# Performance work log

Hardware: AMD Instinct MI355X
Metric: run time of the kernel (lower is better)

Reference implementation:

```python
import jax, jax.numpy as jnp
import numpy as np

B, T, D_MODEL = 2, 2048, 2048
N_HEAD, N_KV = 16, 4
HEAD_DIM = D_MODEL // N_HEAD  # 128
N_REP = N_HEAD // N_KV        # 4
ROPE_BASE = 10000.0


def setup_inputs() -> dict:
    key = jax.random.key(0)
    ks = jax.random.split(key, 5)
    s = 0.02
    return {
        "x": jax.random.normal(ks[0], (B, T, D_MODEL), dtype=jnp.float32),
        "Wq": jax.random.normal(ks[1], (D_MODEL, N_HEAD * HEAD_DIM), dtype=jnp.float32) * s,
        "Wk": jax.random.normal(ks[2], (D_MODEL, N_KV * HEAD_DIM), dtype=jnp.float32) * s,
        "Wv": jax.random.normal(ks[3], (D_MODEL, N_KV * HEAD_DIM), dtype=jnp.float32) * s,
        "Wo": jax.random.normal(ks[4], (D_MODEL, D_MODEL), dtype=jnp.float32) * s,
    }


def _rope_cos_sin(seq_len, dim, dtype):
    inv_freq = 1.0 / (ROPE_BASE ** (jnp.arange(0, dim, 2, dtype=jnp.float32) / dim))
    t = jnp.arange(seq_len, dtype=jnp.float32)
    freqs = t[:, None] * inv_freq[None, :]          # (T, dim/2)
    emb = jnp.concatenate([freqs, freqs], axis=-1)  # (T, dim)
    return jnp.cos(emb).astype(dtype), jnp.sin(emb).astype(dtype)


def _rotate_half(x):
    half = x.shape[-1] // 2
    return jnp.concatenate([-x[..., half:], x[..., :half]], axis=-1)


def reference(x, Wq, Wk, Wv, Wo):
    Bx, Tx, _ = x.shape
    # projections (weights stored (in, out); equals torch Linear with W^T)
    q = (x @ Wq).reshape(Bx, Tx, N_HEAD, HEAD_DIM).transpose(0, 2, 1, 3)  # (B,H,T,d)
    k = (x @ Wk).reshape(Bx, Tx, N_KV, HEAD_DIM).transpose(0, 2, 1, 3)    # (B,Hkv,T,d)
    v = (x @ Wv).reshape(Bx, Tx, N_KV, HEAD_DIM).transpose(0, 2, 1, 3)

    cos, sin = _rope_cos_sin(Tx, HEAD_DIM, x.dtype)  # (T, d)
    q = q * cos + _rotate_half(q) * sin
    k = k * cos + _rotate_half(k) * sin

    # grouped attention: q grouped by kv head, avoids materializing repeated K/V
    qg = q.reshape(Bx, N_KV, N_REP, Tx, HEAD_DIM)
    scale = 1.0 / np.sqrt(HEAD_DIM)
    att = jnp.einsum('bgrtd,bgsd->bgrts', qg, k) * scale  # (B,Hkv,rep,T,S)
    causal = jnp.tril(jnp.ones((Tx, Tx), dtype=bool))
    att = jnp.where(causal, att, -jnp.inf)
    att = jax.nn.softmax(att, axis=-1)
    y = jnp.einsum('bgrts,bgsd->bgrtd', att, v)           # (B,Hkv,rep,T,d)
    y = y.reshape(Bx, N_HEAD, Tx, HEAD_DIM).transpose(0, 2, 1, 3).reshape(Bx, Tx, D_MODEL)
    return y @ Wo
```

## Files before the change

### kernel.cpp

```cpp
#include <hip/hip_runtime.h>
#include <hip/hip_bf16.h>

typedef unsigned short u16;
typedef unsigned int u32;
typedef __attribute__((ext_vector_type(4))) float f32x4;
typedef __attribute__((ext_vector_type(8))) __bf16 bf16x8;

#define B_   2
#define T_   2048
#define DM   2048
#define NH   16
#define NKV  4
#define HD   128

__device__ __forceinline__ u16 f2bf(float f){
    u32 u = __builtin_bit_cast(u32, f);
    u += 0x7FFFu + ((u >> 16) & 1u);
    return (u16)(u >> 16);
}
__device__ __forceinline__ float bf2f(u16 v){
    return __builtin_bit_cast(float, (u32)v << 16);
}

__device__ __forceinline__ float ex2(float x){
    float r; asm("v_exp_f32 %0, %1" : "=v"(r) : "v"(x)); return r;
}

__device__ __forceinline__ void gld_lds16(const void* g, void* l){
    __builtin_amdgcn_global_load_lds(
        (const __attribute__((address_space(1))) void*)g,
        (__attribute__((address_space(3))) void*)l, 16, 0, 0);
}

__global__ void prep(const float* __restrict__ x,
                     const float* __restrict__ Wq, const float* __restrict__ Wk,
                     const float* __restrict__ Wv, const float* __restrict__ Wo,
                     u16* __restrict__ xb, u16* __restrict__ Wqkv, u16* __restrict__ Wot,
                     float2* __restrict__ tab){
    __shared__ float tile[32][33];
    int bid = blockIdx.x, tid = threadIdx.x;
    if (bid < 8192){
        int i = bid * 256 + tid;
        float4 v = ((const float4*)x)[i];
        ushort4 o;
        o.x = f2bf(v.x); o.y = f2bf(v.y); o.z = f2bf(v.z); o.w = f2bf(v.w);
        ((ushort4*)xb)[i] = o;
    } else if (bid < 18432){
        int tb = bid - 8192;
        int bx = tb % 160, byy = tb / 160;
        const float* W; u16* Out; int N; int nb; int perm;
        if (bx < 64)      { W = Wq; Out = Wqkv;                  N = 2048; nb = bx;      perm = 1; }
        else if (bx < 80) { W = Wk; Out = Wqkv + 2048ull * 2048; N = 512;  nb = bx - 64; perm = 1; }
        else if (bx < 96) { W = Wv; Out = Wqkv + 2560ull * 2048; N = 512;  nb = bx - 80; perm = 0; }
        else              { W = Wo; Out = Wot;                   N = 2048; nb = bx - 96; perm = 0; }
        int n0 = nb * 32, k0 = byy * 32;
        int tx = tid & 31, ty = tid >> 5;
#pragma unroll
        for (int i = 0; i < 4; i++)
            tile[ty + i * 8][tx] = W[(size_t)(k0 + ty + i * 8) * N + n0 + tx];
        __syncthreads();
#pragma unroll
        for (int i = 0; i < 4; i++){
            int n = n0 + ty + i * 8;
            int np = perm ? ((n & ~127) | ((n & 63) << 1) | ((n >> 6) & 1)) : n;
            Out[(size_t)np * 2048 + k0 + tx] = f2bf(tile[tx][ty + i * 8]);
        }
    } else {
        int idx = (bid - 18432) * 256 + tid;
        int i = idx & 63, t = idx >> 6;
        float ang = (float)t * exp2f((float)i * (-13.287712379549449f / 64.0f));
        float sv, cv;
        __sincosf(ang, &sv, &cv);
        tab[idx] = make_float2(cv, sv);
    }
}

#define BARR() asm volatile("s_barrier" ::: "memory")
#define VM0()  asm volatile("s_waitcnt vmcnt(0)" ::: "memory")
#define VM4()  asm volatile("s_waitcnt vmcnt(4)" ::: "memory")
#define VM8()  asm volatile("s_waitcnt vmcnt(8)" ::: "memory")
#define VM10() asm volatile("s_waitcnt vmcnt(10)" ::: "memory")

__global__ __launch_bounds__(256, 2) void gemm192h(const u16* __restrict__ A, const u16* __restrict__ Bt,
                                                   u16* __restrict__ Qp, u16* __restrict__ Ktl,
                                                   u16* __restrict__ Vtl, const float2* __restrict__ tab){
    __shared__ __attribute__((aligned(16))) u16 As[2][8192];
    __shared__ __attribute__((aligned(16))) u16 Bs[2][12288];
    const int tid = threadIdx.x;
    const int lane = tid & 63, w = tid >> 6;
    const int wm = w >> 1, wn = w & 1;
    const int tg = lane >> 4, lx = lane & 15;
    int swz = ((int)blockIdx.x & 7) * 64 + ((int)blockIdx.x >> 3);
    const int bx = swz & 15, by = swz >> 4;
    const int m0 = by * 128, n0 = bx * 192;
    const int K = 2048;
    const int kcx = (lane & 7) ^ ((lane >> 3) & 7);

    f32x4 acc[4][6];
    const f32x4 Z = {0.f, 0.f, 0.f, 0.f};
#pragma unroll
    for (int i = 0; i < 4; i++)
#pragma unroll
        for (int j = 0; j < 6; j++) acc[i][j] = Z;
    bf16x8 a_[4][2], b_[2][2];

    auto stA2 = [&](int buf, int h, int kt){
#pragma unroll
        for (int l = 0; l < 2; l++){
            int rb = h * 64 + w * 16 + l * 8;
            gld_lds16(A + (size_t)(m0 + rb + (lane >> 3)) * K + kt * 64 + kcx * 8,
                      &As[buf][rb * 64 + lane * 8]);
        }
    };
    auto stB2 = [&](int buf, int cp, int kt){
#pragma unroll
        for (int l = 0; l < 2; l++){
            int rb = l * 96 + cp * 32 + w * 8;
            gld_lds16(Bt + (size_t)(n0 + rb + (lane >> 3)) * K + kt * 64 + kcx * 8,
                      &Bs[buf][rb * 64 + lane * 8]);
        }
    };

#define RA192(BUF) { \
    const char* ab = (const char*)&As[BUF][0]; \
    _Pragma("unroll") for (int mi = 0; mi < 4; mi++){ \
        int rh = wm*64 + mi*16 + lx; \
        _Pragma("unroll") for (int ks = 0; ks < 2; ks++) \
            a_[mi][ks] = *(const bf16x8*)(ab + rh*128 + (((ks*4+tg)*16) ^ ((lx&7)<<4))); \
    } }
#define RB192(BUF, C) { \
    const char* bb = (const char*)&Bs[BUF][0]; \
    _Pragma("unroll") for (int n = 0; n < 2; n++){ \
        int rb = wn*96 + (C)*32 + n*16 + lx; \
        _Pragma("unroll") for (int ks = 0; ks < 2; ks++) \
            b_[n][ks] = *(const bf16x8*)(bb + rb*128 + (((ks*4+tg)*16) ^ ((lx&7)<<4))); \
    } }
#define MM192(C) { \
    __builtin_amdgcn_s_setprio(1); \
    _Pragma("unroll") for (int mi = 0; mi < 4; mi++) \
    _Pragma("unroll") for (int n = 0; n < 2; n++) \
    _Pragma("unroll") for (int ks = 0; ks < 2; ks++) \
        acc[mi][(C)*2+n] = __builtin_amdgcn_mfma_f32_16x16x32_bf16( \
            a_[mi][ks], b_[n][ks], acc[mi][(C)*2+n], 0, 0, 0); \
    __builtin_amdgcn_s_setprio(0); }

    stA2(0, 0, 0); stA2(0, 1, 0); stB2(0, 0, 0); stB2(0, 1, 0); stB2(0, 2, 0);
    stA2(1, 0, 1); stA2(1, 1, 1); stB2(1, 0, 1); stB2(1, 1, 1);
    VM8(); BARR();

#pragma unroll 1
    for (int it = 0; it < 16; it++){
        const int O  = 2*it + 1;
        const int E2 = (2*it + 2 < 32) ? 2*it + 2 : 31;
        const int O2 = (2*it + 3 < 32) ? 2*it + 3 : 31;
        RA192(0); RB192(0, 0); stB2(1, 2, O);
        BARR(); MM192(0); BARR();
        RB192(0, 1); stA2(0, 0, E2); stB2(0, 0, E2);
        BARR(); MM192(1); BARR();
        RB192(0, 2); stA2(0, 1, E2); stB2(0, 1, E2);
        BARR(); MM192(2); VM10(); BARR();
        RA192(1); RB192(1, 0); stB2(0, 2, E2);
        BARR(); MM192(0); BARR();
        RB192(1, 1); stA2(1, 0, O2); stB2(1, 0, O2);
        BARR(); MM192(1); BARR();
        RB192(1, 2); stA2(1, 1, O2); stB2(1, 1, O2);
        BARR(); MM192(2); VM10(); BARR();
    }

    const float QS = 0.08838834764831845f * 1.4426950408889634f;
#pragma unroll
    for (int mi = 0; mi < 4; mi++){
        int r0 = m0 + wm*64 + mi*16 + tg*4;
#pragma unroll
        for (int ci = 0; ci < 6; ci++){
            int cb = n0 + wn*96 + ci*16;
            int c  = cb + lx;
            if (cb < 2048){
                int ii = (c & 127) >> 1;
#pragma unroll
                for (int j = 0; j < 4; j++){
                    float v = acc[mi][ci][j];
                    float p = __shfl_xor(v, 1);
                    int t = (r0 + j) & 2047;
                    float2 cs = tab[t * 64 + ii];
                    float o = ((lx & 1) ? (v * cs.x + p * cs.y) : (v * cs.x - p * cs.y)) * QS;
                    Qp[(size_t)(r0 + j) * 2048 + c] = f2bf(o);
                }
            } else if (cb < 2560){
                int hk = (c >> 7) & 3;
                int dd = c & 127;
                int ii = dd >> 1;
#pragma unroll
                for (int j = 0; j < 4; j++){
                    int r = r0 + j;
                    int bb2 = r >> 11, tt = r & 2047;
                    float v = acc[mi][ci][j];
                    float p = __shfl_xor(v, 1);
                    float2 cs = tab[tt * 64 + ii];
                    float o = (lx & 1) ? (v * cs.x + p * cs.y) : (v * cs.x - p * cs.y);
                    size_t tb = ((size_t)(bb2 * 4 + hk) * 32 + (tt >> 6)) * 8192;
                    u32 byte = (u32)((tt & 63) * 256) + (((u32)(2 * dd)) ^ ((u32)((tt & 7) << 4)));
                    Ktl[tb + byte / 2] = f2bf(o);
                }
            } else {
                int bb2 = r0 >> 11, ss = r0 & 2047;
                int sb = ss & 63;
                int hk = (c >> 7) & 3;
                int d  = c & 127;
                size_t tb = ((size_t)(bb2 * 4 + hk) * 32 + (ss >> 6)) * 8192;
                u32 swzd = (u32)((d & 7) << 4);
#pragma unroll
                for (int j = 0; j < 4; j++){
                    int s = sb + j;
                    int slot = (s & 32) | (((s >> 2) & 3) << 3) | (((s >> 4) & 1) << 2) | (s & 3);
                    u32 byte = (u32)(d * 128) + (((u32)(2 * slot)) ^ swzd);
                    Vtl[tb + byte / 2] = f2bf(acc[mi][ci][j]);
                }
            }
        }
    }
}
#undef RA192
#undef RB192
#undef MM192

#define READ_A(QA, BUF) { \
    const char* ab = (const char*)&As[BUF][wm][0]; \
    _Pragma("unroll") for (int i = 0; i < 4; i++){ \
        int rh = ((QA)*4 + i)*16 + lx; \
        _Pragma("unroll") for (int ks = 0; ks < 2; ks++) \
            a_[i][ks] = *(const bf16x8*)(ab + rh*128 + (((ks*4+tg)*16) ^ ((lx&7)<<4))); \
    } }
#define READ_B(QB, BUF) { \
    const char* bb = (const char*)&Bs[BUF][wn>>1][0]; \
    _Pragma("unroll") for (int n = 0; n < 2; n++){ \
        int rbh = (wn&1)*64 + ((QB)*2+n)*16 + lx; \
        _Pragma("unroll") for (int ks = 0; ks < 2; ks++) \
            b_[(QB)*2+n][ks] = *(const bf16x8*)(bb + rbh*128 + (((ks*4+tg)*16) ^ ((lx&7)<<4))); \
    } }
#define MFMA_Q(QA, QB) { \
    __builtin_amdgcn_s_setprio(1); \
    _Pragma("unroll") for (int i = 0; i < 4; i++) \
    _Pragma("unroll") for (int n = 0; n < 2; n++) \
    _Pragma("unroll") for (int ks = 0; ks < 2; ks++) \
        acc[(QA)*4+i][(QB)*2+n] = __builtin_amdgcn_mfma_f32_16x16x32_bf16( \
            a_[i][ks], b_[(QB)*2+n][ks], acc[(QA)*4+i][(QB)*2+n], 0, 0, 0); \
    __builtin_amdgcn_s_setprio(0); }

__global__ __launch_bounds__(512, 2) void gemmWo(const u16* __restrict__ A, const u16* __restrict__ Bt,
                                                 u16* __restrict__ O0){
    __shared__ __attribute__((aligned(16))) u16 As[2][2][8192];
    __shared__ __attribute__((aligned(16))) u16 Bs[2][2][8192];
    const int tid = threadIdx.x;
    const int lane = tid & 63, w = tid >> 6;
    const int wm = w >> 2, wn = w & 3;
    const int tg = lane >> 4, lx = lane & 15;
    int q8 = (int)gridDim.x >> 3;
    int swz = ((int)blockIdx.x & 7) * q8 + ((int)blockIdx.x >> 3);
    int kh = swz >> 7; swz &= 127;
    const int bx = swz & 7, by = swz >> 3;
    const int m0 = by * 256, n0 = bx * 256;
    const int K = 2048;
    const int NIT = 8;
    const int kt0 = kh * 16;
    const int ltMax = 2 * NIT - 1;
    const int kcx = (lane & 7) ^ ((lane >> 3) & 7);

    f32x4 acc[8][4];
    const f32x4 Z = {0.f, 0.f, 0.f, 0.f};
#pragma unroll
    for (int i = 0; i < 8; i++)
#pragma unroll
        for (int j = 0; j < 4; j++) acc[i][j] = Z;
    bf16x8 a_[4][2], b_[4][2];

    auto stA = [&](int buf, int q, int kt){
        int mh = w >> 2;
        int s0 = (w & 3) * 2;
#pragma unroll
        for (int l = 0; l < 2; l++){
            int s = s0 + l;
            gld_lds16(A + (size_t)(m0 + mh*128 + q*64 + s*8 + (lane>>3)) * K + kt*64 + kcx*8,
                      &As[buf][mh][q*4096 + s*512 + lane*8]);
        }
    };
    auto stB = [&](int buf, int q, int kt){
        int bh = w >> 2;
        int hi = (w >> 1) & 1;
        int s0 = (w & 1) * 2;
#pragma unroll
        for (int l = 0; l < 2; l++){
            int s = s0 + l;
            gld_lds16(Bt + (size_t)(n0 + bh*128 + hi*64 + q*32 + s*8 + (lane>>3)) * K + kt*64 + kcx*8,
                      &Bs[buf][bh][hi*4096 + q*2048 + s*512 + lane*8]);
        }
    };

    stA(0, 0, kt0); stB(0, 0, kt0); stA(0, 1, kt0); stB(0, 1, kt0);
    stA(1, 0, kt0 + 1); stB(1, 0, kt0 + 1);
    VM4(); BARR();

#pragma unroll 1
    for (int it = 0; it < NIT; it++){
        const int T1 = kt0 + 2*it + 1;
        const int T2 = kt0 + ((2*it + 2 < ltMax) ? 2*it + 2 : ltMax);
        const int T3 = kt0 + ((2*it + 3 < ltMax) ? 2*it + 3 : ltMax);
        READ_A(0, 0); READ_B(0, 0); stA(1, 1, T1);
        BARR(); MFMA_Q(0, 0); BARR();
        READ_B(1, 0); stB(1, 1, T1);
        BARR(); MFMA_Q(0, 1); BARR();
        READ_A(1, 0); stA(0, 0, T2);
        BARR(); MFMA_Q(1, 0); BARR();
        stB(0, 0, T2);
        BARR(); MFMA_Q(1, 1); VM4(); BARR();
        READ_A(0, 1); READ_B(0, 1); stA(0, 1, T2);
        BARR(); MFMA_Q(0, 0); BARR();
        READ_B(1, 1); stB(0, 1, T2);
        BARR(); MFMA_Q(0, 1); BARR();
        READ_A(1, 1); stA(1, 0, T3);
        BARR(); MFMA_Q(1, 0); BARR();
        stB(1, 0, T3);
        BARR(); MFMA_Q(1, 1); VM4(); BARR();
    }

    u16* C = O0 + (size_t)kh * 4096 * 2048;
#pragma unroll
    for (int mi = 0; mi < 8; mi++)
#pragma unroll
        for (int ni = 0; ni < 4; ni++){
            int r0 = m0 + wm*128 + mi*16 + tg*4;
            int c  = n0 + wn*64 + ni*16 + lx;
#pragma unroll
            for (int j = 0; j < 4; j++)
                C[(size_t)(r0 + j) * 2048 + c] = f2bf(acc[mi][ni][j]);
        }
}

__global__ void reduceWo(const u16* __restrict__ P, float* __restrict__ out){
    size_t t = (size_t)blockIdx.x * 256 + threadIdx.x;
    const u16* p0 = P + t * 8;
    const u16* p1 = P + 4096ull * 2048 + t * 8;
    uint4 a = *(const uint4*)p0;
    uint4 b = *(const uint4*)p1;
    const u16* as = (const u16*)&a;
    const u16* bs = (const u16*)&b;
    float4 o0, o1;
    o0.x = bf2f(as[0]) + bf2f(bs[0]); o0.y = bf2f(as[1]) + bf2f(bs[1]);
    o0.z = bf2f(as[2]) + bf2f(bs[2]); o0.w = bf2f(as[3]) + bf2f(bs[3]);
    o1.x = bf2f(as[4]) + bf2f(bs[4]); o1.y = bf2f(as[5]) + bf2f(bs[5]);
    o1.z = bf2f(as[6]) + bf2f(bs[6]); o1.w = bf2f(as[7]) + bf2f(bs[7]);
    ((float4*)out)[t * 2]     = o0;
    ((float4*)out)[t * 2 + 1] = o1;
}

__global__ __launch_bounds__(256) void attn9(const u16* __restrict__ Q, const u16* __restrict__ Kt,
                                             const u16* __restrict__ Vt, u16* __restrict__ Y){
    __shared__ __attribute__((aligned(16))) u16 Ks[8192];
    __shared__ __attribute__((aligned(16))) u16 Vs[8192];
    const int tid = threadIdx.x;
    const int lane = tid & 63, w = tid >> 6;
    const int tg = lane >> 4, lx = lane & 15;
    int gid = blockIdx.x;
    int z = gid & 255, k4 = gid >> 8;
    int j8 = z & 7, h = (z >> 3) & 15, b = z >> 7;
    int qt = (k4 == 0) ? j8 : (k4 == 1) ? 31 - j8 : (k4 == 2) ? j8 + 8 : 23 - j8;
    const int hkv = h >> 2;
    const size_t kvBase = ((size_t)(b * NKV + hkv) * 32) * 8192;
    const f32x4 Z = {0.f, 0.f, 0.f, 0.f};

    auto STAGE_K = [&](int it){
        const u16* kg = Kt + kvBase + (size_t)it * 8192;
#pragma unroll
        for (int i = 0; i < 4; i++){
            int is = w * 4 + i;
            gld_lds16(kg + is * 512 + lane * 8, &Ks[is * 512]);
        }
    };
    auto STAGE_V = [&](int it){
        const u16* vg = Vt + kvBase + (size_t)it * 8192;
#pragma unroll
        for (int i = 0; i < 4; i++){
            int is = w * 4 + i;
            gld_lds16(vg + is * 512 + lane * 8, &Vs[is * 512]);
        }
    };

    const int q0 = qt * 64;
    const int qrow = q0 + w * 16 + lx;
    bf16x8 qfr[4];
#pragma unroll
    for (int kk = 0; kk < 4; kk++)
        qfr[kk] = *(const bf16x8*)(Q + (size_t)(b * T_ + qrow) * DM + h * HD + kk * 32 + tg * 8);
    f32x4 accO[8];
#pragma unroll
    for (int i = 0; i < 8; i++) accO[i] = Z;
    float mr = -INFINITY;
    float lp = 0.f;
    const int nIter = qt + 1;

    STAGE_K(0); STAGE_V(0);

#pragma unroll 1
    for (int it = 0; it < nIter; it++){
        const bool last = (it + 1 == nIter);
        VM4(); BARR();
        f32x4 sa[4];
#pragma unroll
        for (int c = 0; c < 4; c++) sa[c] = Z;
        __builtin_amdgcn_s_setprio(1);
#pragma unroll
        for (int c = 0; c < 4; c++){
            int s = c * 16 + lx;
            u32 swz = (u32)((s & 7) << 4);
            const char* kb = (const char*)&Ks[0] + s * 256;
#pragma unroll
            for (int kk = 0; kk < 4; kk++){
                bf16x8 kf = *(const bf16x8*)(kb + (((u32)(kk * 64 + tg * 16)) ^ swz));
                sa[c] = __builtin_amdgcn_mfma_f32_16x16x32_bf16(kf, qfr[kk], sa[c], 0, 0, 0);
            }
        }
        __builtin_amdgcn_s_setprio(0);
        BARR();
        if (!last) STAGE_K(it + 1);
        const int sBase = it * 64 + tg * 4;
        float tl = -INFINITY;
#pragma unroll
        for (int c = 0; c < 4; c++){
#pragma unroll
            for (int j = 0; j < 4; j++){
                float a = sa[c][j];
                if (last){
                    if (sBase + c * 16 + j > qrow) a = -INFINITY;
                }
                sa[c][j] = a;
                tl = fmaxf(tl, a);
            }
        }
        if (!__all(tl <= mr + 8.f)){
            float t = fmaxf(tl, __shfl_xor(tl, 16));
            t = fmaxf(t, __shfl_xor(t, 32));
            float mn = fmaxf(mr, t);
            float corrq = ex2(mr - mn);
            mr = mn;
            lp *= corrq;
            float corrO[4];
#pragma unroll
            for (int j = 0; j < 4; j++)
                corrO[j] = __shfl(corrq, (lane & 48) + ((lane >> 4) << 2) + j);
#pragma unroll
            for (int dt = 0; dt < 8; dt++){
                f32x4 t2 = accO[dt];
                t2[0] *= corrO[0]; t2[1] *= corrO[1]; t2[2] *= corrO[2]; t2[3] *= corrO[3];
                accO[dt] = t2;
            }
        }
        float p[4][4];
#pragma unroll
        for (int c = 0; c < 4; c++)
#pragma unroll
            for (int j = 0; j < 4; j++){
                float v = ex2(sa[c][j] - mr);
                p[c][j] = v;
                lp += v;
            }
        bf16x8 pa0, pa1;
        {
            u32 w0, w1, w2, w3;
            asm("v_cvt_pk_bf16_f32 %0, %1, %2" : "=v"(w0) : "v"(p[0][0]), "v"(p[0][1]));
            asm("v_cvt_pk_bf16_f32 %0, %1, %2" : "=v"(w1) : "v"(p[0][2]), "v"(p[0][3]));
            asm("v_cvt_pk_bf16_f32 %0, %1, %2" : "=v"(w2) : "v"(p[1][0]), "v"(p[1][1]));
            asm("v_cvt_pk_bf16_f32 %0, %1, %2" : "=v"(w3) : "v"(p[1][2]), "v"(p[1][3]));
            u32 r[4] = {w0, w1, w2, w3};
            pa0 = __builtin_bit_cast(bf16x8, *(uint4*)r);
            asm("v_cvt_pk_bf16_f32 %0, %1, %2" : "=v"(w0) : "v"(p[2][0]), "v"(p[2][1]));
            asm("v_cvt_pk_bf16_f32 %0, %1, %2" : "=v"(w1) : "v"(p[2][2]), "v"(p[2][3]));
            asm("v_cvt_pk_bf16_f32 %0, %1, %2" : "=v"(w2) : "v"(p[3][0]), "v"(p[3][1]));
            asm("v_cvt_pk_bf16_f32 %0, %1, %2" : "=v"(w3) : "v"(p[3][2]), "v"(p[3][3]));
            u32 r2[4] = {w0, w1, w2, w3};
            pa1 = __builtin_bit_cast(bf16x8, *(uint4*)r2);
        }
        if (last){ VM0(); } else { VM4(); }
        BARR();
        __builtin_amdgcn_s_setprio(1);
#pragma unroll
        for (int dt = 0; dt < 8; dt++){
            int d = dt * 16 + lx;
            u32 swz = (u32)((d & 7) << 4);
            const char* vb = (const char*)&Vs[0] + d * 128;
            bf16x8 vf0 = *(const bf16x8*)(vb + (((u32)(tg * 16))      ^ swz));
            bf16x8 vf1 = *(const bf16x8*)(vb + (((u32)(tg * 16 + 64)) ^ swz));
            accO[dt] = __builtin_amdgcn_mfma_f32_16x16x32_bf16(pa0, vf0, accO[dt], 0, 0, 0);
            accO[dt] = __builtin_amdgcn_mfma_f32_16x16x32_bf16(pa1, vf1, accO[dt], 0, 0, 0);
        }
        __builtin_amdgcn_s_setprio(0);
        BARR();
        if (!last) STAGE_V(it + 1);
    }
    lp += __shfl_xor(lp, 16);
    lp += __shfl_xor(lp, 32);
    float invq = 1.0f / lp;
    float inv[4];
#pragma unroll
    for (int j = 0; j < 4; j++)
        inv[j] = __shfl(invq, (lane & 48) + ((lane >> 4) << 2) + j);
#pragma unroll
    for (int dt = 0; dt < 8; dt++)
#pragma unroll
        for (int j = 0; j < 4; j++){
            int qr = q0 + w * 16 + tg * 4 + j;
            int d = dt * 16 + lx;
            Y[(size_t)(b * T_ + qr) * DM + h * HD + d] = f2bf(accO[dt][j] * inv[j]);
        }
}

extern "C" void kernel_launch(void* const* d_in, const int* in_sizes, int n_in,
                              void* d_out, int out_size, void* d_ws, size_t ws_size,
                              hipStream_t stream){
    const float* x  = (const float*)d_in[0];
    const float* Wq = (const float*)d_in[1];
    const float* Wk = (const float*)d_in[2];
    const float* Wv = (const float*)d_in[3];
    const float* Wo = (const float*)d_in[4];

    char* ws = (char*)d_ws;
    size_t off = 0;
    auto alloc = [&](size_t bytes){ void* p = ws + off; off += (bytes + 255) & ~255ull; return p; };
    u16*    xb   = (u16*)alloc(4096ull * 2048 * 2);
    u16*    Wqkv = (u16*)alloc(3072ull * 2048 * 2);
    u16*    Wot  = (u16*)alloc(2048ull * 2048 * 2);
    u16*    qbb  = (u16*)alloc(4096ull * 2048 * 2);
    u16*    ktl  = (u16*)alloc(2ull * 4 * 32 * 8192 * 2);
    u16*    vtl  = (u16*)alloc(2ull * 4 * 32 * 8192 * 2);
    u16*    ybb  = (u16*)alloc(4096ull * 2048 * 2);
    u16*    pbb  = (u16*)alloc(2ull * 4096 * 2048 * 2);
    float2* tab  = (float2*)alloc(2048ull * 64 * 8);

    prep<<<18944, 256, 0, stream>>>(x, Wq, Wk, Wv, Wo, xb, Wqkv, Wot, tab);

    gemm192h<<<512, 256, 0, stream>>>(xb, Wqkv, qbb, ktl, vtl, tab);

    attn9<<<1024, 256, 0, stream>>>(qbb, ktl, vtl, ybb);

    gemmWo<<<256, 512, 0, stream>>>(ybb, Wot, pbb);
    reduceWo<<<4096, 256, 0, stream>>>(pbb, (float*)d_out);
}
```

Measured before the change: 183.8 us.

## Replace 128x192 double-buffered QKV GEMM with 128x96 single-buffer tile kernel

The QKV projection GEMM moves from a 128x192 tile with a double-buffered, finely interleaved LDS pipeline to a 128x96 tile with one LDS buffer. Each K step issues the next stage's global-to-LDS loads after the fragments are read into registers. Launch bounds rise to 4 blocks per CU and the grid doubles to 1024 blocks, aiming for more occupancy and better load balance across CUs. The cost is less data reuse per tile, more total global/L2 traffic, and a full vmcnt(0) wait plus barrier each iteration, which exposes load latency except where other resident blocks hide it.

```diff
diff --git a/kernel.cpp b/kernel.cpp
--- a/kernel.cpp
+++ b/kernel.cpp
@@ -78,102 +78,89 @@
 #define BARR() asm volatile("s_barrier" ::: "memory")
 #define VM0()  asm volatile("s_waitcnt vmcnt(0)" ::: "memory")
 #define VM4()  asm volatile("s_waitcnt vmcnt(4)" ::: "memory")
-#define VM8()  asm volatile("s_waitcnt vmcnt(8)" ::: "memory")
-#define VM10() asm volatile("s_waitcnt vmcnt(10)" ::: "memory")
-
-__global__ __launch_bounds__(256, 2) void gemm192h(const u16* __restrict__ A, const u16* __restrict__ Bt,
-                                                   u16* __restrict__ Qp, u16* __restrict__ Ktl,
-                                                   u16* __restrict__ Vtl, const float2* __restrict__ tab){
-    __shared__ __attribute__((aligned(16))) u16 As[2][8192];
-    __shared__ __attribute__((aligned(16))) u16 Bs[2][12288];
+#define LGKM0() asm volatile("s_waitcnt lgkmcnt(0)" ::: "memory")
+
+__global__ __launch_bounds__(256, 4) void gemm96(const u16* __restrict__ A, const u16* __restrict__ Bt,
+                                                 u16* __restrict__ Qp, u16* __restrict__ Ktl,
+                                                 u16* __restrict__ Vtl, const float2* __restrict__ tab){
+    __shared__ __attribute__((aligned(16))) u16 As[8192];
+    __shared__ __attribute__((aligned(16))) u16 Bs[6144];
     const int tid = threadIdx.x;
     const int lane = tid & 63, w = tid >> 6;
     const int wm = w >> 1, wn = w & 1;
     const int tg = lane >> 4, lx = lane & 15;
-    int swz = ((int)blockIdx.x & 7) * 64 + ((int)blockIdx.x >> 3);
-    const int bx = swz & 15, by = swz >> 4;
-    const int m0 = by * 128, n0 = bx * 192;
+    int swz = ((int)blockIdx.x & 7) * 128 + ((int)blockIdx.x >> 3);
+    const int bx = swz & 31, by = swz >> 5;
+    const int m0 = by * 128, n0 = bx * 96;
     const int K = 2048;
     const int kcx = (lane & 7) ^ ((lane >> 3) & 7);
 
-    f32x4 acc[4][6];
+    f32x4 acc[4][3];
     const f32x4 Z = {0.f, 0.f, 0.f, 0.f};
 #pragma unroll
     for (int i = 0; i < 4; i++)
 #pragma unroll
-        for (int j = 0; j < 6; j++) acc[i][j] = Z;
-    bf16x8 a_[4][2], b_[2][2];
-
-    auto stA2 = [&](int buf, int h, int kt){
-#pragma unroll
-        for (int l = 0; l < 2; l++){
-            int rb = h * 64 + w * 16 + l * 8;
-            gld_lds16(A + (size_t)(m0 + rb + (lane >> 3)) * K + kt * 64 + kcx * 8,
-                      &As[buf][rb * 64 + lane * 8]);
+        for (int j = 0; j < 3; j++) acc[i][j] = Z;
+    bf16x8 a_[4][2], b_[3][2];
+
+    auto stage = [&](int kt){
+#pragma unroll
+        for (int s = 0; s < 4; s++){
+            int rb = s * 32 + w * 8 + (lane >> 3);
+            gld_lds16(A + (size_t)(m0 + rb) * K + kt * 64 + kcx * 8,
+                      &As[rb * 64 + lane * 8]);
+        }
+#pragma unroll
+        for (int s = 0; s < 3; s++){
+            int rb = s * 32 + w * 8 + (lane >> 3);
+            gld_lds16(Bt + (size_t)(n0 + rb) * K + kt * 64 + kcx * 8,
+                      &Bs[rb * 64 + lane * 8]);
         }
     };
-    auto stB2 = [&](int buf, int cp, int kt){
-#pragma unroll
-        for (int l = 0; l < 2; l++){
-            int rb = l * 96 + cp * 32 + w * 8;
-            gld_lds16(Bt + (size_t)(n0 + rb + (lane >> 3)) * K + kt * 64 + kcx * 8,
-                      &Bs[buf][rb * 64 + lane * 8]);
-        }
-    };
-
-#define RA192(BUF) { \
-    const char* ab = (const char*)&As[BUF][0]; \
-    _Pragma("unroll") for (int mi = 0; mi < 4; mi++){ \
-        int rh = wm*64 + mi*16 + lx; \
-        _Pragma("unroll") for (int ks = 0; ks < 2; ks++) \
-            a_[mi][ks] = *(const bf16x8*)(ab + rh*128 + (((ks*4+tg)*16) ^ ((lx&7)<<4))); \
-    } }
-#define RB192(BUF, C) { \
-    const char* bb = (const char*)&Bs[BUF][0]; \
-    _Pragma("unroll") for (int n = 0; n < 2; n++){ \
-        int rb = wn*96 + (C)*32 + n*16 + lx; \
-        _Pragma("unroll") for (int ks = 0; ks < 2; ks++) \
-            b_[n][ks] = *(const bf16x8*)(bb + rb*128 + (((ks*4+tg)*16) ^ ((lx&7)<<4))); \
-    } }
-#define MM192(C) { \
-    __builtin_amdgcn_s_setprio(1); \
-    _Pragma("unroll") for (int mi = 0; mi < 4; mi++) \
-    _Pragma("unroll") for (int n = 0; n < 2; n++) \
-    _Pragma("unroll") for (int ks = 0; ks < 2; ks++) \
-        acc[mi][(C)*2+n] = __builtin_amdgcn_mfma_f32_16x16x32_bf16( \
-            a_[mi][ks], b_[n][ks], acc[mi][(C)*2+n], 0, 0, 0); \
-    __builtin_amdgcn_s_setprio(0); }
-
-    stA2(0, 0, 0); stA2(0, 1, 0); stB2(0, 0, 0); stB2(0, 1, 0); stB2(0, 2, 0);
-    stA2(1, 0, 1); stA2(1, 1, 1); stB2(1, 0, 1); stB2(1, 1, 1);
-    VM8(); BARR();
+
+    stage(0);
 
 #pragma unroll 1
-    for (int it = 0; it < 16; it++){
-        const int O  = 2*it + 1;
-        const int E2 = (2*it + 2 < 32) ? 2*it + 2 : 31;
-        const int O2 = (2*it + 3 < 32) ? 2*it + 3 : 31;
-        RA192(0); RB192(0, 0); stB2(1, 2, O);
-        BARR(); MM192(0); BARR();
-        RB192(0, 1); stA2(0, 0, E2); stB2(0, 0, E2);
-        BARR(); MM192(1); BARR();
-        RB192(0, 2); stA2(0, 1, E2); stB2(0, 1, E2);
-        BARR(); MM192(2); VM10(); BARR();
-        RA192(1); RB192(1, 0); stB2(0, 2, E2);
-        BARR(); MM192(0); BARR();
-        RB192(1, 1); stA2(1, 0, O2); stB2(1, 0, O2);
-        BARR(); MM192(1); BARR();
-        RB192(1, 2); stA2(1, 1, O2); stB2(1, 1, O2);
-        BARR(); MM192(2); VM10(); BARR();
+    for (int kt = 0; kt < 32; kt++){
+        VM0(); BARR();
+#pragma unroll
+        for (int mi = 0; mi < 4; mi++){
+            int rh = wm * 64 + mi * 16 + lx;
+#pragma unroll
+            for (int ks = 0; ks < 2; ks++)
+                a_[mi][ks] = *(const bf16x8*)((const char*)As + rh * 128 +
+                              (((ks * 4 + tg) * 16) ^ ((lx & 7) << 4)));
+        }
+#pragma unroll
+        for (int ci = 0; ci < 3; ci++){
+            int rb = wn * 48 + ci * 16 + lx;
+#pragma unroll
+            for (int ks = 0; ks < 2; ks++)
+                b_[ci][ks] = *(const bf16x8*)((const char*)Bs + rb * 128 +
+                              (((ks * 4 + tg) * 16) ^ ((lx & 7) << 4)));
+        }
+        LGKM0();
+        BARR();
+        if (kt + 1 < 32) stage(kt + 1);
+        __builtin_amdgcn_s_setprio(1);
+#pragma unroll
+        for (int mi = 0; mi < 4; mi++)
+#pragma unroll
+            for (int ci = 0; ci < 3; ci++)
+#pragma unroll
+                for (int ks = 0; ks < 2; ks++)
+                    acc[mi][ci] = __builtin_amdgcn_mfma_f32_16x16x32_bf16(
+                        a_[mi][ks], b_[ci][ks], acc[mi][ci], 0, 0, 0);
+        __builtin_amdgcn_s_setprio(0);
     }
 
     const float QS = 0.08838834764831845f * 1.4426950408889634f;
 #pragma unroll
     for (int mi = 0; mi < 4; mi++){
-        int r0 = m0 + wm*64 + mi*16 + tg*4;
-#pragma unroll
-        for (int ci = 0; ci < 6; ci++){
-            int cb = n0 + wn*96 + ci*16;
+        int r0 = m0 + wm * 64 + mi * 16 + tg * 4;
+#pragma unroll
+        for (int ci = 0; ci < 3; ci++){
+            int cb = n0 + wn * 48 + ci * 16;
             int c  = cb + lx;
             if (cb < 2048){
                 int ii = (c & 127) >> 1;
@@ -220,9 +207,6 @@
         }
     }
 }
-#undef RA192
-#undef RB192
-#undef MM192
 
 #define READ_A(QA, BUF) { \
     const char* ab = (const char*)&As[BUF][wm][0]; \
@@ -537,7 +521,7 @@
 
     prep<<<18944, 256, 0, stream>>>(x, Wq, Wk, Wv, Wo, xb, Wqkv, Wot, tab);
 
-    gemm192h<<<512, 256, 0, stream>>>(xb, Wqkv, qbb, ktl, vtl, tab);
+    gemm96<<<1024, 256, 0, stream>>>(xb, Wqkv, qbb, ktl, vtl, tab);
 
     attn9<<<1024, 256, 0, stream>>>(qbb, ktl, vtl, ybb);
 
```

Result: slower. 195.1 us (+6.1%).

## Software-pipeline attention: overlap next QK^T MFMAs with current softmax

Applied to the files above, without the earlier changes.

Restructures the attention loop so the QK^T for tile i is computed in the same phase as the softmax of tile i-1. Two score register sets are ping-ponged, and the loop is unrolled by two with a masked tail step. The aim is to let the MFMA work and the exp/max VALU work interleave, hiding the softmax latency. The cost is more register pressure, which could lower occupancy, and a reordered K/V staging and barrier sequence.

```diff
diff --git a/kernel.cpp b/kernel.cpp
--- a/kernel.cpp
+++ b/kernel.cpp
@@ -353,8 +353,8 @@
     ((float4*)out)[t * 2 + 1] = o1;
 }
 
-__global__ __launch_bounds__(256) void attn9(const u16* __restrict__ Q, const u16* __restrict__ Kt,
-                                             const u16* __restrict__ Vt, u16* __restrict__ Y){
+__global__ __launch_bounds__(256) void attn11(const u16* __restrict__ Q, const u16* __restrict__ Kt,
+                                              const u16* __restrict__ Vt, u16* __restrict__ Y){
     __shared__ __attribute__((aligned(16))) u16 Ks[8192];
     __shared__ __attribute__((aligned(16))) u16 Vs[8192];
     const int tid = threadIdx.x;
@@ -396,106 +396,121 @@
     for (int i = 0; i < 8; i++) accO[i] = Z;
     float mr = -INFINITY;
     float lp = 0.f;
-    const int nIter = qt + 1;
-
-    STAGE_K(0); STAGE_V(0);
-
+    const int n = qt + 1;
+
+    f32x4 saA[4], saB[4];
+    bf16x8 pa0, pa1;
+
+#define QK16(SA) { \
+    _Pragma("unroll") for (int c = 0; c < 4; c++) SA[c] = Z; \
+    _Pragma("unroll") for (int c = 0; c < 4; c++){ \
+        int s = c * 16 + lx; \
+        u32 kswz = (u32)((s & 7) << 4); \
+        const char* kb = (const char*)&Ks[0] + s * 256; \
+        _Pragma("unroll") for (int kk = 0; kk < 4; kk++){ \
+            bf16x8 kf = *(const bf16x8*)(kb + (((u32)(kk * 64 + tg * 16)) ^ kswz)); \
+            SA[c] = __builtin_amdgcn_mfma_f32_16x16x32_bf16(kf, qfr[kk], SA[c], 0, 0, 0); \
+        } } }
+
+#define SM16(SP, MASKED, LI) { \
+    float tl = -INFINITY; \
+    _Pragma("unroll") for (int c = 0; c < 4; c++) \
+    _Pragma("unroll") for (int j = 0; j < 4; j++){ \
+        float a = SP[c][j]; \
+        if (MASKED){ if ((LI) * 64 + tg * 4 + c * 16 + j > qrow) a = -INFINITY; } \
+        SP[c][j] = a; \
+        tl = fmaxf(tl, a); } \
+    if (!__all(tl <= mr + 8.f)){ \
+        float t = fmaxf(tl, __shfl_xor(tl, 16)); \
+        t = fmaxf(t, __shfl_xor(t, 32)); \
+        float mn = fmaxf(mr, t); \
+        float corrq = ex2(mr - mn); \
+        mr = mn; lp *= corrq; \
+        float corrO[4]; \
+        _Pragma("unroll") for (int j = 0; j < 4; j++) \
+            corrO[j] = __shfl(corrq, (lane & 48) + ((lane >> 4) << 2) + j); \
+        _Pragma("unroll") for (int dt = 0; dt < 8; dt++){ \
+            f32x4 t2 = accO[dt]; \
+            t2[0] *= corrO[0]; t2[1] *= corrO[1]; t2[2] *= corrO[2]; t2[3] *= corrO[3]; \
+            accO[dt] = t2; } } \
+    { float pp[4][4]; \
+      _Pragma("unroll") for (int c = 0; c < 4; c++) \
+      _Pragma("unroll") for (int j = 0; j < 4; j++){ \
+          float v = ex2(SP[c][j] - mr); pp[c][j] = v; lp += v; } \
+      u32 w0, w1, w2, w3; \
+      asm("v_cvt_pk_bf16_f32 %0, %1, %2" : "=v"(w0) : "v"(pp[0][0]), "v"(pp[0][1])); \
+      asm("v_cvt_pk_bf16_f32 %0, %1, %2" : "=v"(w1) : "v"(pp[0][2]), "v"(pp[0][3])); \
+      asm("v_cvt_pk_bf16_f32 %0, %1, %2" : "=v"(w2) : "v"(pp[1][0]), "v"(pp[1][1])); \
+      asm("v_cvt_pk_bf16_f32 %0, %1, %2" : "=v"(w3) : "v"(pp[1][2]), "v"(pp[1][3])); \
+      u32 r1[4] = {w0, w1, w2, w3}; \
+      pa0 = __builtin_bit_cast(bf16x8, *(uint4*)r1); \
+      asm("v_cvt_pk_bf16_f32 %0, %1, %2" : "=v"(w0) : "v"(pp[2][0]), "v"(pp[2][1])); \
+      asm("v_cvt_pk_bf16_f32 %0, %1, %2" : "=v"(w1) : "v"(pp[2][2]), "v"(pp[2][3])); \
+      asm("v_cvt_pk_bf16_f32 %0, %1, %2" : "=v"(w2) : "v"(pp[3][0]), "v"(pp[3][1])); \
+      asm("v_cvt_pk_bf16_f32 %0, %1, %2" : "=v"(w3) : "v"(pp[3][2]), "v"(pp[3][3])); \
+      u32 r2[4] = {w0, w1, w2, w3}; \
+      pa1 = __builtin_bit_cast(bf16x8, *(uint4*)r2); } }
+
+#define PV16() { \
+    _Pragma("unroll") for (int dt = 0; dt < 8; dt++){ \
+        int d = dt * 16 + lx; \
+        u32 vswz = (u32)((d & 7) << 4); \
+        const char* vb = (const char*)&Vs[0] + d * 128; \
+        bf16x8 vf0 = *(const bf16x8*)(vb + (((u32)(tg * 16))      ^ vswz)); \
+        bf16x8 vf1 = *(const bf16x8*)(vb + (((u32)(tg * 16 + 64)) ^ vswz)); \
+        accO[dt] = __builtin_amdgcn_mfma_f32_16x16x32_bf16(pa0, vf0, accO[dt], 0, 0, 0); \
+        accO[dt] = __builtin_amdgcn_mfma_f32_16x16x32_bf16(pa1, vf1, accO[dt], 0, 0, 0); } }
+
+#define AFULL(SC, SP, I) { \
+    VM4(); BARR(); \
+    __builtin_amdgcn_s_setprio(1); \
+    QK16(SC); \
+    SM16(SP, false, 0); \
+    __builtin_amdgcn_s_setprio(0); \
+    BARR(); \
+    if ((I) + 1 < n){ STAGE_K((I) + 1); VM4(); } else { VM0(); } \
+    BARR(); \
+    __builtin_amdgcn_s_setprio(1); \
+    PV16(); \
+    __builtin_amdgcn_s_setprio(0); \
+    BARR(); \
+    STAGE_V(I); }
+
+#define ATAIL(SP, LI) { \
+    VM0(); BARR(); \
+    SM16(SP, true, LI); \
+    __builtin_amdgcn_s_setprio(1); \
+    PV16(); \
+    __builtin_amdgcn_s_setprio(0); }
+
+    STAGE_K(0);
+    VM0(); BARR();
+    __builtin_amdgcn_s_setprio(1);
+    QK16(saA);
+    __builtin_amdgcn_s_setprio(0);
+    BARR();
+    if (n > 1) STAGE_K(1);
+    STAGE_V(0);
+
+    int i = 1;
 #pragma unroll 1
-    for (int it = 0; it < nIter; it++){
-        const bool last = (it + 1 == nIter);
-        VM4(); BARR();
-        f32x4 sa[4];
-#pragma unroll
-        for (int c = 0; c < 4; c++) sa[c] = Z;
-        __builtin_amdgcn_s_setprio(1);
-#pragma unroll
-        for (int c = 0; c < 4; c++){
-            int s = c * 16 + lx;
-            u32 swz = (u32)((s & 7) << 4);
-            const char* kb = (const char*)&Ks[0] + s * 256;
-#pragma unroll
-            for (int kk = 0; kk < 4; kk++){
-                bf16x8 kf = *(const bf16x8*)(kb + (((u32)(kk * 64 + tg * 16)) ^ swz));
-                sa[c] = __builtin_amdgcn_mfma_f32_16x16x32_bf16(kf, qfr[kk], sa[c], 0, 0, 0);
-            }
-        }
-        __builtin_amdgcn_s_setprio(0);
-        BARR();
-        if (!last) STAGE_K(it + 1);
-        const int sBase = it * 64 + tg * 4;
-        float tl = -INFINITY;
-#pragma unroll
-        for (int c = 0; c < 4; c++){
-#pragma unroll
-            for (int j = 0; j < 4; j++){
-                float a = sa[c][j];
-                if (last){
-                    if (sBase + c * 16 + j > qrow) a = -INFINITY;
-                }
-                sa[c][j] = a;
-                tl = fmaxf(tl, a);
-            }
-        }
-        if (!__all(tl <= mr + 8.f)){
-            float t = fmaxf(tl, __shfl_xor(tl, 16));
-            t = fmaxf(t, __shfl_xor(t, 32));
-            float mn = fmaxf(mr, t);
-            float corrq = ex2(mr - mn);
-            mr = mn;
-            lp *= corrq;
-            float corrO[4];
-#pragma unroll
-            for (int j = 0; j < 4; j++)
-                corrO[j] = __shfl(corrq, (lane & 48) + ((lane >> 4) << 2) + j);
-#pragma unroll
-            for (int dt = 0; dt < 8; dt++){
-                f32x4 t2 = accO[dt];
-                t2[0] *= corrO[0]; t2[1] *= corrO[1]; t2[2] *= corrO[2]; t2[3] *= corrO[3];
-                accO[dt] = t2;
-            }
-        }
-        float p[4][4];
-#pragma unroll
-        for (int c = 0; c < 4; c++)
-#pragma unroll
-            for (int j = 0; j < 4; j++){
-                float v = ex2(sa[c][j] - mr);
-                p[c][j] = v;
-                lp += v;
-            }
-        bf16x8 pa0, pa1;
-        {
-            u32 w0, w1, w2, w3;
-            asm("v_cvt_pk_bf16_f32 %0, %1, %2" : "=v"(w0) : "v"(p[0][0]), "v"(p[0][1]));
-            asm("v_cvt_pk_bf16_f32 %0, %1, %2" : "=v"(w1) : "v"(p[0][2]), "v"(p[0][3]));
-            asm("v_cvt_pk_bf16_f32 %0, %1, %2" : "=v"(w2) : "v"(p[1][0]), "v"(p[1][1]));
-            asm("v_cvt_pk_bf16_f32 %0, %1, %2" : "=v"(w3) : "v"(p[1][2]), "v"(p[1][3]));
-            u32 r[4] = {w0, w1, w2, w3};
-            pa0 = __builtin_bit_cast(bf16x8, *(uint4*)r);
-            asm("v_cvt_pk_bf16_f32 %0, %1, %2" : "=v"(w0) : "v"(p[2][0]), "v"(p[2][1]));
-            asm("v_cvt_pk_bf16_f32 %0, %1, %2" : "=v"(w1) : "v"(p[2][2]), "v"(p[2][3]));
-            asm("v_cvt_pk_bf16_f32 %0, %1, %2" : "=v"(w2) : "v"(p[3][0]), "v"(p[3][1]));
-            asm("v_cvt_pk_bf16_f32 %0, %1, %2" : "=v"(w3) : "v"(p[3][2]), "v"(p[3][3]));
-            u32 r2[4] = {w0, w1, w2, w3};
-            pa1 = __builtin_bit_cast(bf16x8, *(uint4*)r2);
-        }
-        if (last){ VM0(); } else { VM4(); }
-        BARR();
-        __builtin_amdgcn_s_setprio(1);
-#pragma unroll
-        for (int dt = 0; dt < 8; dt++){
-            int d = dt * 16 + lx;
-            u32 swz = (u32)((d & 7) << 4);
-            const char* vb = (const char*)&Vs[0] + d * 128;
-            bf16x8 vf0 = *(const bf16x8*)(vb + (((u32)(tg * 16))      ^ swz));
-            bf16x8 vf1 = *(const bf16x8*)(vb + (((u32)(tg * 16 + 64)) ^ swz));
-            accO[dt] = __builtin_amdgcn_mfma_f32_16x16x32_bf16(pa0, vf0, accO[dt], 0, 0, 0);
-            accO[dt] = __builtin_amdgcn_mfma_f32_16x16x32_bf16(pa1, vf1, accO[dt], 0, 0, 0);
-        }
-        __builtin_amdgcn_s_setprio(0);
-        BARR();
-        if (!last) STAGE_V(it + 1);
+    for (; i + 1 < n; i += 2){
+        AFULL(saB, saA, i);
+        AFULL(saA, saB, i + 1);
     }
+    if (i < n){
+        AFULL(saB, saA, i);
+        ATAIL(saB, n - 1);
+    } else {
+        ATAIL(saA, n - 1);
+    }
+
+#undef QK16
+#undef SM16
+#undef PV16
+#undef AFULL
+#undef ATAIL
+
     lp += __shfl_xor(lp, 16);
     lp += __shfl_xor(lp, 32);
     float invq = 1.0f / lp;
@@ -539,7 +554,7 @@
 
     gemm192h<<<512, 256, 0, stream>>>(xb, Wqkv, qbb, ktl, vtl, tab);
 
-    attn9<<<1024, 256, 0, stream>>>(qbb, ktl, vtl, ybb);
+    attn11<<<1024, 256, 0, stream>>>(qbb, ktl, vtl, ybb);
 
     gemmWo<<<256, 512, 0, stream>>>(ybb, Wot, pbb);
     reduceWo<<<4096, 256, 0, stream>>>(pbb, (float*)d_out);
```

New measurement: 194.7 us. 1.06x slower.
